# Kernel tuning notes

Hardware: AMD Instinct MI355X
Metric: run time of the kernel (lower is better)

The kernel has to match this reference:

```python
import jax, jax.numpy as jnp
import numpy as np


def setup_inputs() -> dict:
    key = jax.random.key(0)
    ks = jax.random.split(key, 10)
    B, N, K, F, H, C, L = 2, 20000, 32, 128, 128, 40, 3
    return {
        "vertex_feat": jax.random.uniform(ks[0], (B, N, F), dtype=jnp.float32),
        "neighbors_idx": jax.random.randint(ks[1], (B, N, K), 0, N, dtype=jnp.int32),
        "valid_lens": jax.random.randint(ks[2], (B, N), 0, K + 1, dtype=jnp.int32),
        "W_embed": jax.random.normal(ks[3], (F, H), dtype=jnp.float32) * 0.05,
        "gcn_W": jax.random.normal(ks[4], (L, H, H), dtype=jnp.float32) * 0.05,
        "gcn_B": jax.random.normal(ks[5], (L, H, H), dtype=jnp.float32) * 0.05,
        "cls_W1": jax.random.normal(ks[6], (H, H), dtype=jnp.float32) * 0.05,
        "cls_b1": jnp.zeros((H,), dtype=jnp.float32),
        "cls_W2": jax.random.normal(ks[7], (H, C), dtype=jnp.float32) * 0.05,
        "cls_b2": jnp.zeros((C,), dtype=jnp.float32),
    }


def reference(vertex_feat, neighbors_idx, valid_lens, W_embed, gcn_W, gcn_B,
              cls_W1, cls_b1, cls_W2, cls_b2):
    # --- input embedding: Dense(no bias) / row-sum of raw features ---
    row_sum = jnp.sum(vertex_feat, axis=-1, keepdims=True)          # [B,N,1]
    h = jnp.einsum('bnf,fh->bnh', vertex_feat, W_embed) / row_sum   # [B,N,H]

    # valid_lens with zeros replaced by 1, as float divisor
    vl = jnp.where(valid_lens == 0, 1, valid_lens)
    vl = vl.astype(jnp.float32)[..., None]                          # [B,N,1]

    num_layers = gcn_W.shape[0]
    for l in range(num_layers):
        # gather-sum neighbor features (per-graph gather, batch_dims=1)
        neigh = jax.vmap(lambda feat, idx: feat[idx])(h, neighbors_idx)  # [B,N,K,H]
        neigh = jnp.sum(neigh, axis=2) / vl                              # [B,N,H]
        h = jax.nn.relu(jnp.einsum('bnh,hd->bnd', neigh, gcn_W[l])
                        + jnp.einsum('bnh,hd->bnd', h, gcn_B[l]))

    # --- classifier MLP (dropout inactive at inference) ---
    z = jax.nn.relu(jnp.einsum('bnh,hd->bnd', h, cls_W1) + cls_b1)
    logits = jnp.einsum('bnd,dc->bnc', z, cls_W2) + cls_b2
    return jax.nn.softmax(logits, axis=-1)
```

## Files before the change

kernel.cpp:

```cpp
#include <hip/hip_runtime.h>
#include <hip/hip_bf16.h>

typedef __hip_bfloat16 bf16;
typedef __attribute__((ext_vector_type(8))) short short8;
typedef __attribute__((ext_vector_type(4))) float f32x4;

#define NB    20000
#define BATCH 2
#define HDIM  128
#define KNBR  32
#define NCLS  40
#define NLAYER 3
#define BM    64
#define LBM   32
#define LDP   136
#define NTILES 625
#define LTPH   625
#define LGRID  1256

__device__ __forceinline__ short f2bf(float v) {
    return __builtin_bit_cast(short, __float2bfloat16(v));
}
__device__ __forceinline__ float blo(unsigned u) { return __builtin_bit_cast(float, u << 16); }
__device__ __forceinline__ float bhi(unsigned u) { return __builtin_bit_cast(float, u & 0xffff0000u); }

__global__ void pack_weights(const float* __restrict__ Wemb, const float* __restrict__ gW,
                             const float* __restrict__ gB, const float* __restrict__ W1,
                             const float* __restrict__ W2, short* __restrict__ pw) {
    const int idx = blockIdx.x * 256 + threadIdx.x;
    if (idx < 8 * 16384) {
        const int m = idx >> 14, e = idx & 16383;
        const float* src = (m == 0) ? Wemb
                         : (m <= 3) ? gW + (size_t)(m - 1) * 16384
                         : (m <= 6) ? gB + (size_t)(m - 4) * 16384
                         : W1;
        const int k = e >> 7, n = e & 127;
        pw[m * 16384 + (((k >> 3) * 128 + n) << 3) + (k & 7)] = f2bf(src[e]);
    } else {
        const int e = idx - 8 * 16384;
        if (e < 128 * NCLS) {
            const int k = e / NCLS, n = e - k * NCLS;
            pw[8 * 16384 + ((k >> 3) * NCLS + n) * 8 + (k & 7)] = f2bf(W2[e]);
        }
    }
}

__global__ __launch_bounds__(512, 4) void embed_gemm(const float* __restrict__ x,
                                                     const short* __restrict__ pwE,
                                                     bf16* __restrict__ h0) {
    __shared__ short sx[BM * LDP];
    const int t = threadIdx.x;
    const int row0 = blockIdx.x * BM;

    {
        const int r = t >> 3, fs = (t & 7) * 16;
        const float4* p = (const float4*)(x + (size_t)(row0 + r) * HDIM + fs);
        float4 v[4];
#pragma unroll
        for (int i = 0; i < 4; ++i) v[i] = p[i];
        const float* vf = (const float*)v;
        unsigned* dst = (unsigned*)(sx + r * LDP + fs);
#pragma unroll
        for (int i = 0; i < 8; ++i) {
            unsigned lo = (unsigned)(unsigned short)f2bf(vf[2 * i]);
            unsigned hi = (unsigned)(unsigned short)f2bf(vf[2 * i + 1]);
            dst[i] = lo | (hi << 16);
        }
    }
    __syncthreads();

    const int w = t >> 6, l = t & 63;
    const int m16 = l & 15, quad = l >> 4;
    const int col = w * 16 + m16;

    short8 ones;
#pragma unroll
    for (int j = 0; j < 8; ++j) ones[j] = (short)0x3F80;

    short8 wf[4];
#pragma unroll
    for (int q = 0; q < 4; ++q)
        wf[q] = *(const short8*)(pwE + (((q * 4 + quad) * 128 + col) << 3));

    f32x4 acc[4] = {}, rsum[4] = {};
#pragma unroll
    for (int q = 0; q < 4; ++q)
#pragma unroll
        for (int mt = 0; mt < 4; ++mt) {
            short8 a = *(const short8*)(sx + (mt * 16 + m16) * LDP + q * 32 + quad * 8);
            acc[mt]  = __builtin_amdgcn_mfma_f32_16x16x32_bf16(a, wf[q], acc[mt], 0, 0, 0);
            rsum[mt] = __builtin_amdgcn_mfma_f32_16x16x32_bf16(a, ones,  rsum[mt], 0, 0, 0);
        }

#pragma unroll
    for (int mt = 0; mt < 4; ++mt)
#pragma unroll
        for (int r = 0; r < 4; ++r) {
            const int rr = row0 + mt * 16 + quad * 4 + r;
            h0[(size_t)rr * HDIM + col] = __float2bfloat16(acc[mt][r] / rsum[mt][r]);
        }
}

__global__ __launch_bounds__(256, 6) void layer_gemm(const bf16* __restrict__ h_in,
                                                     const int* __restrict__ nidx,
                                                     const int* __restrict__ vlen,
                                                     const short* __restrict__ pwW,
                                                     const short* __restrict__ pwB,
                                                     bf16* __restrict__ h_out) {
    __shared__ int   sidx[LBM * KNBR];
    __shared__ short sng[LBM * LDP];
    __shared__ short sh[LBM * LDP];

    const int slot = blockIdx.x & 7;
    const int half = slot >> 2;
    const int idx  = (blockIdx.x >> 3) * 4 + (slot & 3);
    if (idx >= LTPH) return;
    const int tile = half * LTPH + idx;

    const int t = threadIdx.x;
    const int row0 = tile * LBM;

    ((int4*)sidx)[t] = ((const int4*)(nidx + (size_t)row0 * KNBR))[t];
    {
        const int r = t >> 3, fs = (t & 7) * 16;
        const uint4* p = (const uint4*)(h_in + (size_t)(row0 + r) * HDIM + fs);
        uint4 a = p[0], b = p[1];
        uint4* d = (uint4*)(sh + r * LDP + fs);
        d[0] = a; d[1] = b;
    }
    __syncthreads();

    {
        const int node = t >> 3;
        const int fs8 = (t & 7) * 8;
        const int g = row0 + node;
        const bf16* hb = h_in + (size_t)((g >= NB) ? NB : 0) * HDIM;
        const int* ip = sidx + node * KNBR;
        int vl = vlen[g]; if (vl == 0) vl = 1;
        const float inv = 1.0f / (float)vl;

#pragma unroll
        for (int fh = 0; fh < 2; ++fh) {
            const int fs = fh * 64 + fs8;
            float acc[8];
#pragma unroll
            for (int i = 0; i < 8; ++i) acc[i] = 0.0f;
#pragma unroll 4
            for (int k = 0; k < KNBR; ++k) {
                const uint4 u = *(const uint4*)(hb + (size_t)ip[k] * HDIM + fs);
                acc[0] += blo(u.x); acc[1] += bhi(u.x);
                acc[2] += blo(u.y); acc[3] += bhi(u.y);
                acc[4] += blo(u.z); acc[5] += bhi(u.z);
                acc[6] += blo(u.w); acc[7] += bhi(u.w);
            }
            unsigned* dst = (unsigned*)(sng + node * LDP + fs);
#pragma unroll
            for (int i = 0; i < 4; ++i) {
                unsigned lo = (unsigned)(unsigned short)f2bf(acc[2 * i] * inv);
                unsigned hi = (unsigned)(unsigned short)f2bf(acc[2 * i + 1] * inv);
                dst[i] = lo | (hi << 16);
            }
            __syncthreads();
        }
    }

    const int w = t >> 6, l = t & 63;
    const int m16 = l & 15, quad = l >> 4;
    const int ncol0 = w * 32;

    f32x4 acc[2][2] = {};
#pragma unroll
    for (int q = 0; q < 4; ++q) {
        short8 wfW[2], wfB[2];
#pragma unroll
        for (int nt = 0; nt < 2; ++nt) {
            const int off = ((q * 4 + quad) * 128 + ncol0 + nt * 16 + m16) << 3;
            wfW[nt] = *(const short8*)(pwW + off);
            wfB[nt] = *(const short8*)(pwB + off);
        }
#pragma unroll
        for (int mt = 0; mt < 2; ++mt) {
            short8 aN = *(const short8*)(sng + (mt * 16 + m16) * LDP + q * 32 + quad * 8);
            short8 aH = *(const short8*)(sh  + (mt * 16 + m16) * LDP + q * 32 + quad * 8);
#pragma unroll
            for (int nt = 0; nt < 2; ++nt) {
                acc[mt][nt] = __builtin_amdgcn_mfma_f32_16x16x32_bf16(aN, wfW[nt], acc[mt][nt], 0, 0, 0);
                acc[mt][nt] = __builtin_amdgcn_mfma_f32_16x16x32_bf16(aH, wfB[nt], acc[mt][nt], 0, 0, 0);
            }
        }
    }

#pragma unroll
    for (int mt = 0; mt < 2; ++mt)
#pragma unroll
        for (int nt = 0; nt < 2; ++nt)
#pragma unroll
            for (int r = 0; r < 4; ++r) {
                const int rr = row0 + mt * 16 + quad * 4 + r;
                const int cc = ncol0 + nt * 16 + m16;
                h_out[(size_t)rr * HDIM + cc] = __float2bfloat16(fmaxf(acc[mt][nt][r], 0.0f));
            }
}

__global__ __launch_bounds__(512, 4) void cls_gemm(const bf16* __restrict__ h,
                                                   const short* __restrict__ pwW1,
                                                   const float* __restrict__ b1,
                                                   const short* __restrict__ pwW2,
                                                   const float* __restrict__ b2,
                                                   float* __restrict__ out) {
    __shared__ short sh[BM * LDP];
    __shared__ short sz[BM * LDP];
    __shared__ float lg[BM * 48];
    const int t = threadIdx.x;
    const int row0 = blockIdx.x * BM;

    {
        const int r = t >> 3, fs = (t & 7) * 16;
        const uint4* p = (const uint4*)(h + (size_t)(row0 + r) * HDIM + fs);
        uint4 a = p[0], b = p[1];
        uint4* d = (uint4*)(sh + r * LDP + fs);
        d[0] = a; d[1] = b;
    }
    __syncthreads();

    const int w = t >> 6, l = t & 63;
    const int m16 = l & 15, quad = l >> 4;
    const int col = w * 16 + m16;

    {
        short8 wf[4];
#pragma unroll
        for (int q = 0; q < 4; ++q)
            wf[q] = *(const short8*)(pwW1 + (((q * 4 + quad) * 128 + col) << 3));
        f32x4 acc[4] = {};
#pragma unroll
        for (int q = 0; q < 4; ++q)
#pragma unroll
            for (int mt = 0; mt < 4; ++mt) {
                short8 a = *(const short8*)(sh + (mt * 16 + m16) * LDP + q * 32 + quad * 8);
                acc[mt] = __builtin_amdgcn_mfma_f32_16x16x32_bf16(a, wf[q], acc[mt], 0, 0, 0);
            }
        const float bias = b1[col];
#pragma unroll
        for (int mt = 0; mt < 4; ++mt)
#pragma unroll
            for (int r = 0; r < 4; ++r)
                sz[(mt * 16 + quad * 4 + r) * LDP + col] = f2bf(fmaxf(acc[mt][r] + bias, 0.0f));
    }
    __syncthreads();

    if (w < 3) {
        const bool valid = (col < NCLS);
        short8 wf[4];
#pragma unroll
        for (int q = 0; q < 4; ++q) {
            if (valid) wf[q] = *(const short8*)(pwW2 + (((q * 4 + quad) * NCLS + col) << 3));
            else {
#pragma unroll
                for (int j = 0; j < 8; ++j) wf[q][j] = 0;
            }
        }
        f32x4 acc[4] = {};
#pragma unroll
        for (int q = 0; q < 4; ++q)
#pragma unroll
            for (int mt = 0; mt < 4; ++mt) {
                short8 a = *(const short8*)(sz + (mt * 16 + m16) * LDP + q * 32 + quad * 8);
                acc[mt] = __builtin_amdgcn_mfma_f32_16x16x32_bf16(a, wf[q], acc[mt], 0, 0, 0);
            }
        if (valid) {
            const float bias = b2[col];
#pragma unroll
            for (int mt = 0; mt < 4; ++mt)
#pragma unroll
                for (int r = 0; r < 4; ++r)
                    lg[(mt * 16 + quad * 4 + r) * 48 + col] = acc[mt][r] + bias;
        }
    }
    __syncthreads();

    if (t < BM) {
        float* row = lg + t * 48;
        float m = row[0];
        for (int c = 1; c < NCLS; ++c) m = fmaxf(m, row[c]);
        float s = 0.0f;
        for (int c = 0; c < NCLS; ++c) { float e = expf(row[c] - m); row[c] = e; s += e; }
        const float inv = 1.0f / s;
        for (int c = 0; c < NCLS; ++c) row[c] *= inv;
    }
    __syncthreads();

    for (int i = t; i < BM * NCLS; i += 512) {
        const int r = i / NCLS, c = i - r * NCLS;
        out[(size_t)row0 * NCLS + i] = lg[r * 48 + c];
    }
}

extern "C" void kernel_launch(void* const* d_in, const int* in_sizes, int n_in,
                              void* d_out, int out_size, void* d_ws, size_t ws_size,
                              hipStream_t stream) {
    const float* x    = (const float*)d_in[0];
    const int*  nidx  = (const int*)  d_in[1];
    const int*  vlen  = (const int*)  d_in[2];
    const float* Wemb = (const float*)d_in[3];
    const float* gW   = (const float*)d_in[4];
    const float* gB   = (const float*)d_in[5];
    const float* W1   = (const float*)d_in[6];
    const float* b1   = (const float*)d_in[7];
    const float* W2   = (const float*)d_in[8];
    const float* b2   = (const float*)d_in[9];
    float* out = (float*)d_out;

    const int nodes = BATCH * NB;
    bf16* h0 = (bf16*)d_ws;
    bf16* h1 = h0 + (size_t)nodes * HDIM;
    short* pw = (short*)(h1 + (size_t)nodes * HDIM);
    const short* pwE  = pw;
    const short* pwW1 = pw + 7 * 16384;
    const short* pwW2 = pw + 8 * 16384;

    pack_weights<<<(8 * 16384 + 128 * NCLS + 255) / 256, 256, 0, stream>>>(Wemb, gW, gB, W1, W2, pw);
    embed_gemm<<<NTILES, 512, 0, stream>>>(x, pwE, h0);

    for (int lyr = 0; lyr < NLAYER; ++lyr) {
        layer_gemm<<<LGRID, 256, 0, stream>>>(h0, nidx, vlen,
                                              pw + (size_t)(1 + lyr) * 16384,
                                              pw + (size_t)(4 + lyr) * 16384,
                                              h1);
        bf16* tmp = h0; h0 = h1; h1 = tmp;
    }

    cls_gemm<<<NTILES, 512, 0, stream>>>(h0, pwW1, b1, pwW2, b2, out);
}
```

Baseline: 169.3 us.

## Fuse weight packing into embed kernel and fuse last GCN layer with classifier

Merges the weight-packing kernel into the embedding GEMM: extra blocks pack the weights, and the embed blocks read and convert W_embed directly from fp32. It also fuses the third GCN layer with the classifier MLP and softmax in one 32-row-tile kernel, so the final hidden state never goes to global memory. This removes two kernel launches and one full write and read of the node features. In exchange the embed blocks do strided fp32 weight loads, and the fused kernel holds more shared memory per block, which may lower occupancy.

```diff
diff --git a/kernel.cpp b/kernel.cpp
--- a/kernel.cpp
+++ b/kernel.cpp
@@ -6,17 +6,17 @@
 typedef __attribute__((ext_vector_type(4))) float f32x4;
 
 #define NB    20000
-#define BATCH 2
 #define HDIM  128
 #define KNBR  32
 #define NCLS  40
-#define NLAYER 3
 #define BM    64
 #define LBM   32
 #define LDP   136
 #define NTILES 625
 #define LTPH   625
 #define LGRID  1256
+#define PACKN  (8*16384 + 128*NCLS)
+#define EGRID  (NTILES + 64)
 
 __device__ __forceinline__ short f2bf(float v) {
     return __builtin_bit_cast(short, __float2bfloat16(v));
@@ -24,34 +24,37 @@
 __device__ __forceinline__ float blo(unsigned u) { return __builtin_bit_cast(float, u << 16); }
 __device__ __forceinline__ float bhi(unsigned u) { return __builtin_bit_cast(float, u & 0xffff0000u); }
 
-__global__ void pack_weights(const float* __restrict__ Wemb, const float* __restrict__ gW,
-                             const float* __restrict__ gB, const float* __restrict__ W1,
-                             const float* __restrict__ W2, short* __restrict__ pw) {
-    const int idx = blockIdx.x * 256 + threadIdx.x;
-    if (idx < 8 * 16384) {
-        const int m = idx >> 14, e = idx & 16383;
-        const float* src = (m == 0) ? Wemb
-                         : (m <= 3) ? gW + (size_t)(m - 1) * 16384
-                         : (m <= 6) ? gB + (size_t)(m - 4) * 16384
-                         : W1;
-        const int k = e >> 7, n = e & 127;
-        pw[m * 16384 + (((k >> 3) * 128 + n) << 3) + (k & 7)] = f2bf(src[e]);
-    } else {
-        const int e = idx - 8 * 16384;
-        if (e < 128 * NCLS) {
-            const int k = e / NCLS, n = e - k * NCLS;
-            pw[8 * 16384 + ((k >> 3) * NCLS + n) * 8 + (k & 7)] = f2bf(W2[e]);
-        }
-    }
-}
-
-__global__ __launch_bounds__(512, 4) void embed_gemm(const float* __restrict__ x,
-                                                     const short* __restrict__ pwE,
-                                                     bf16* __restrict__ h0) {
+__global__ __launch_bounds__(512, 4) void embed_pack(const float* __restrict__ x,
+                                                     const float* __restrict__ Wemb,
+                                                     const float* __restrict__ gW,
+                                                     const float* __restrict__ gB,
+                                                     const float* __restrict__ W1,
+                                                     const float* __restrict__ W2,
+                                                     bf16* __restrict__ h0,
+                                                     short* __restrict__ pw) {
+    const int t = threadIdx.x;
+
+    if (blockIdx.x >= NTILES) {
+        for (int idx = (blockIdx.x - NTILES) * 512 + t; idx < PACKN; idx += 64 * 512) {
+            if (idx < 8 * 16384) {
+                const int m = idx >> 14, e = idx & 16383;
+                const float* src = (m == 0) ? Wemb
+                                 : (m <= 3) ? gW + (size_t)(m - 1) * 16384
+                                 : (m <= 6) ? gB + (size_t)(m - 4) * 16384
+                                 : W1;
+                const int k = e >> 7, n = e & 127;
+                pw[m * 16384 + (((k >> 3) * 128 + n) << 3) + (k & 7)] = f2bf(src[e]);
+            } else {
+                const int e = idx - 8 * 16384;
+                const int k = e / NCLS, n = e - k * NCLS;
+                pw[8 * 16384 + ((k >> 3) * NCLS + n) * 8 + (k & 7)] = f2bf(W2[e]);
+            }
+        }
+        return;
+    }
+
     __shared__ short sx[BM * LDP];
-    const int t = threadIdx.x;
     const int row0 = blockIdx.x * BM;
-
     {
         const int r = t >> 3, fs = (t & 7) * 16;
         const float4* p = (const float4*)(x + (size_t)(row0 + r) * HDIM + fs);
@@ -79,8 +82,12 @@
 
     short8 wf[4];
 #pragma unroll
-    for (int q = 0; q < 4; ++q)
-        wf[q] = *(const short8*)(pwE + (((q * 4 + quad) * 128 + col) << 3));
+    for (int q = 0; q < 4; ++q) {
+        const int kb = q * 32 + quad * 8;
+#pragma unroll
+        for (int j = 0; j < 8; ++j)
+            wf[q][j] = f2bf(Wemb[(kb + j) * HDIM + col]);
+    }
 
     f32x4 acc[4] = {}, rsum[4] = {};
 #pragma unroll
@@ -202,84 +209,173 @@
             }
 }
 
-__global__ __launch_bounds__(512, 4) void cls_gemm(const bf16* __restrict__ h,
-                                                   const short* __restrict__ pwW1,
-                                                   const float* __restrict__ b1,
-                                                   const short* __restrict__ pwW2,
-                                                   const float* __restrict__ b2,
-                                                   float* __restrict__ out) {
-    __shared__ short sh[BM * LDP];
-    __shared__ short sz[BM * LDP];
-    __shared__ float lg[BM * 48];
+__global__ __launch_bounds__(256, 4) void layer3_cls(const bf16* __restrict__ h_in,
+                                                     const int* __restrict__ nidx,
+                                                     const int* __restrict__ vlen,
+                                                     const short* __restrict__ pwW,
+                                                     const short* __restrict__ pwB,
+                                                     const short* __restrict__ pwW1,
+                                                     const float* __restrict__ b1,
+                                                     const short* __restrict__ pwW2,
+                                                     const float* __restrict__ b2,
+                                                     float* __restrict__ out) {
+    __shared__ int   sidx[LBM * KNBR];
+    __shared__ short sng[LBM * LDP];
+    __shared__ short sh[LBM * LDP];
+    __shared__ float lg[LBM * 48];
+
+    const int slot = blockIdx.x & 7;
+    const int half = slot >> 2;
+    const int idx  = (blockIdx.x >> 3) * 4 + (slot & 3);
+    if (idx >= LTPH) return;
+    const int tile = half * LTPH + idx;
+
     const int t = threadIdx.x;
-    const int row0 = blockIdx.x * BM;
-
+    const int row0 = tile * LBM;
+
+    ((int4*)sidx)[t] = ((const int4*)(nidx + (size_t)row0 * KNBR))[t];
     {
         const int r = t >> 3, fs = (t & 7) * 16;
-        const uint4* p = (const uint4*)(h + (size_t)(row0 + r) * HDIM + fs);
+        const uint4* p = (const uint4*)(h_in + (size_t)(row0 + r) * HDIM + fs);
         uint4 a = p[0], b = p[1];
         uint4* d = (uint4*)(sh + r * LDP + fs);
         d[0] = a; d[1] = b;
     }
     __syncthreads();
 
+    {
+        const int node = t >> 3;
+        const int fs8 = (t & 7) * 8;
+        const int g = row0 + node;
+        const bf16* hb = h_in + (size_t)((g >= NB) ? NB : 0) * HDIM;
+        const int* ip = sidx + node * KNBR;
+        int vl = vlen[g]; if (vl == 0) vl = 1;
+        const float inv = 1.0f / (float)vl;
+
+#pragma unroll
+        for (int fh = 0; fh < 2; ++fh) {
+            const int fs = fh * 64 + fs8;
+            float acc[8];
+#pragma unroll
+            for (int i = 0; i < 8; ++i) acc[i] = 0.0f;
+#pragma unroll 4
+            for (int k = 0; k < KNBR; ++k) {
+                const uint4 u = *(const uint4*)(hb + (size_t)ip[k] * HDIM + fs);
+                acc[0] += blo(u.x); acc[1] += bhi(u.x);
+                acc[2] += blo(u.y); acc[3] += bhi(u.y);
+                acc[4] += blo(u.z); acc[5] += bhi(u.z);
+                acc[6] += blo(u.w); acc[7] += bhi(u.w);
+            }
+            unsigned* dst = (unsigned*)(sng + node * LDP + fs);
+#pragma unroll
+            for (int i = 0; i < 4; ++i) {
+                unsigned lo = (unsigned)(unsigned short)f2bf(acc[2 * i] * inv);
+                unsigned hi = (unsigned)(unsigned short)f2bf(acc[2 * i + 1] * inv);
+                dst[i] = lo | (hi << 16);
+            }
+            __syncthreads();
+        }
+    }
+
     const int w = t >> 6, l = t & 63;
     const int m16 = l & 15, quad = l >> 4;
-    const int col = w * 16 + m16;
-
-    {
-        short8 wf[4];
-#pragma unroll
-        for (int q = 0; q < 4; ++q)
-            wf[q] = *(const short8*)(pwW1 + (((q * 4 + quad) * 128 + col) << 3));
-        f32x4 acc[4] = {};
-#pragma unroll
-        for (int q = 0; q < 4; ++q)
-#pragma unroll
-            for (int mt = 0; mt < 4; ++mt) {
+    const int ncol0 = w * 32;
+
+    f32x4 acc[2][2] = {};
+#pragma unroll
+    for (int q = 0; q < 4; ++q) {
+        short8 wfW[2], wfB[2];
+#pragma unroll
+        for (int nt = 0; nt < 2; ++nt) {
+            const int off = ((q * 4 + quad) * 128 + ncol0 + nt * 16 + m16) << 3;
+            wfW[nt] = *(const short8*)(pwW + off);
+            wfB[nt] = *(const short8*)(pwB + off);
+        }
+#pragma unroll
+        for (int mt = 0; mt < 2; ++mt) {
+            short8 aN = *(const short8*)(sng + (mt * 16 + m16) * LDP + q * 32 + quad * 8);
+            short8 aH = *(const short8*)(sh  + (mt * 16 + m16) * LDP + q * 32 + quad * 8);
+#pragma unroll
+            for (int nt = 0; nt < 2; ++nt) {
+                acc[mt][nt] = __builtin_amdgcn_mfma_f32_16x16x32_bf16(aN, wfW[nt], acc[mt][nt], 0, 0, 0);
+                acc[mt][nt] = __builtin_amdgcn_mfma_f32_16x16x32_bf16(aH, wfB[nt], acc[mt][nt], 0, 0, 0);
+            }
+        }
+    }
+    __syncthreads();
+
+#pragma unroll
+    for (int mt = 0; mt < 2; ++mt)
+#pragma unroll
+        for (int nt = 0; nt < 2; ++nt)
+#pragma unroll
+            for (int r = 0; r < 4; ++r) {
+                const int lr = mt * 16 + quad * 4 + r;
+                const int cc = ncol0 + nt * 16 + m16;
+                sh[lr * LDP + cc] = f2bf(fmaxf(acc[mt][nt][r], 0.0f));
+            }
+    __syncthreads();
+
+    {
+        f32x4 zacc[2][2] = {};
+#pragma unroll
+        for (int q = 0; q < 4; ++q) {
+            short8 wf[2];
+#pragma unroll
+            for (int nt = 0; nt < 2; ++nt)
+                wf[nt] = *(const short8*)(pwW1 + (((q * 4 + quad) * 128 + ncol0 + nt * 16 + m16) << 3));
+#pragma unroll
+            for (int mt = 0; mt < 2; ++mt) {
                 short8 a = *(const short8*)(sh + (mt * 16 + m16) * LDP + q * 32 + quad * 8);
-                acc[mt] = __builtin_amdgcn_mfma_f32_16x16x32_bf16(a, wf[q], acc[mt], 0, 0, 0);
-            }
-        const float bias = b1[col];
-#pragma unroll
-        for (int mt = 0; mt < 4; ++mt)
-#pragma unroll
-            for (int r = 0; r < 4; ++r)
-                sz[(mt * 16 + quad * 4 + r) * LDP + col] = f2bf(fmaxf(acc[mt][r] + bias, 0.0f));
+#pragma unroll
+                for (int nt = 0; nt < 2; ++nt)
+                    zacc[mt][nt] = __builtin_amdgcn_mfma_f32_16x16x32_bf16(a, wf[nt], zacc[mt][nt], 0, 0, 0);
+            }
+        }
+        __syncthreads();
+#pragma unroll
+        for (int nt = 0; nt < 2; ++nt) {
+            const int cc = ncol0 + nt * 16 + m16;
+            const float bias = b1[cc];
+#pragma unroll
+            for (int mt = 0; mt < 2; ++mt)
+#pragma unroll
+                for (int r = 0; r < 4; ++r)
+                    sng[(mt * 16 + quad * 4 + r) * LDP + cc] = f2bf(fmaxf(zacc[mt][nt][r] + bias, 0.0f));
+        }
     }
     __syncthreads();
 
     if (w < 3) {
+        const int col = w * 16 + m16;
         const bool valid = (col < NCLS);
-        short8 wf[4];
+        f32x4 lacc[2] = {};
 #pragma unroll
         for (int q = 0; q < 4; ++q) {
-            if (valid) wf[q] = *(const short8*)(pwW2 + (((q * 4 + quad) * NCLS + col) << 3));
+            short8 wf;
+            if (valid) wf = *(const short8*)(pwW2 + (((q * 4 + quad) * NCLS + col) << 3));
             else {
 #pragma unroll
-                for (int j = 0; j < 8; ++j) wf[q][j] = 0;
-            }
-        }
-        f32x4 acc[4] = {};
-#pragma unroll
-        for (int q = 0; q < 4; ++q)
-#pragma unroll
-            for (int mt = 0; mt < 4; ++mt) {
-                short8 a = *(const short8*)(sz + (mt * 16 + m16) * LDP + q * 32 + quad * 8);
-                acc[mt] = __builtin_amdgcn_mfma_f32_16x16x32_bf16(a, wf[q], acc[mt], 0, 0, 0);
-            }
+                for (int j = 0; j < 8; ++j) wf[j] = 0;
+            }
+#pragma unroll
+            for (int mt = 0; mt < 2; ++mt) {
+                short8 a = *(const short8*)(sng + (mt * 16 + m16) * LDP + q * 32 + quad * 8);
+                lacc[mt] = __builtin_amdgcn_mfma_f32_16x16x32_bf16(a, wf, lacc[mt], 0, 0, 0);
+            }
+        }
         if (valid) {
             const float bias = b2[col];
 #pragma unroll
-            for (int mt = 0; mt < 4; ++mt)
+            for (int mt = 0; mt < 2; ++mt)
 #pragma unroll
                 for (int r = 0; r < 4; ++r)
-                    lg[(mt * 16 + quad * 4 + r) * 48 + col] = acc[mt][r] + bias;
-        }
-    }
-    __syncthreads();
-
-    if (t < BM) {
+                    lg[(mt * 16 + quad * 4 + r) * 48 + col] = lacc[mt][r] + bias;
+        }
+    }
+    __syncthreads();
+
+    if (t < LBM) {
         float* row = lg + t * 48;
         float m = row[0];
         for (int c = 1; c < NCLS; ++c) m = fmaxf(m, row[c]);
@@ -290,7 +386,7 @@
     }
     __syncthreads();
 
-    for (int i = t; i < BM * NCLS; i += 512) {
+    for (int i = t; i < LBM * NCLS; i += 256) {
         const int r = i / NCLS, c = i - r * NCLS;
         out[(size_t)row0 * NCLS + i] = lg[r * 48 + c];
     }
@@ -311,24 +407,18 @@
     const float* b2   = (const float*)d_in[9];
     float* out = (float*)d_out;
 
-    const int nodes = BATCH * NB;
+    const int nodes = 40000;
     bf16* h0 = (bf16*)d_ws;
     bf16* h1 = h0 + (size_t)nodes * HDIM;
     short* pw = (short*)(h1 + (size_t)nodes * HDIM);
-    const short* pwE  = pw;
     const short* pwW1 = pw + 7 * 16384;
     const short* pwW2 = pw + 8 * 16384;
 
-    pack_weights<<<(8 * 16384 + 128 * NCLS + 255) / 256, 256, 0, stream>>>(Wemb, gW, gB, W1, W2, pw);
-    embed_gemm<<<NTILES, 512, 0, stream>>>(x, pwE, h0);
-
-    for (int lyr = 0; lyr < NLAYER; ++lyr) {
-        layer_gemm<<<LGRID, 256, 0, stream>>>(h0, nidx, vlen,
-                                              pw + (size_t)(1 + lyr) * 16384,
-                                              pw + (size_t)(4 + lyr) * 16384,
-                                              h1);
-        bf16* tmp = h0; h0 = h1; h1 = tmp;
-    }
-
-    cls_gemm<<<NTILES, 512, 0, stream>>>(h0, pwW1, b1, pwW2, b2, out);
+    embed_pack<<<EGRID, 512, 0, stream>>>(x, Wemb, gW, gB, W1, W2, h0, pw);
+
+    layer_gemm<<<LGRID, 256, 0, stream>>>(h0, nidx, vlen, pw + 1 * 16384, pw + 4 * 16384, h1);
+    layer_gemm<<<LGRID, 256, 0, stream>>>(h1, nidx, vlen, pw + 2 * 16384, pw + 5 * 16384, h0);
+
+    layer3_cls<<<LGRID, 256, 0, stream>>>(h0, nidx, vlen, pw + 3 * 16384, pw + 6 * 16384,
+                                          pwW1, b1, pwW2, b2, out);
 }
```

Result: faster. 161.5 us, median of 2 (-4.6%).
